# Optimization experiments

Hardware: AMD Instinct MI355X
Metric: run time of the kernel (lower is better)

## Reference

```python
import jax, jax.numpy as jnp
import numpy as np

N, K, A = 4096, 64, 8      # nodes, level-2 paths per node, attrs per l2-neighbor
D = 128                    # embed_dim
NU, NR, NA = 100000, 32, 5000  # user vocab, rating vocab, attribute vocab


def setup_inputs() -> dict:
    key = jax.random.key(0)
    ks = jax.random.split(key, 12)
    s = 0.02
    return dict(
        nodes=jax.random.randint(ks[0], (N,), 0, NU),
        paths_rel=jax.random.randint(ks[1], (N, K, 2), 0, NR),
        paths_nbr=jax.random.randint(ks[2], (N, K), 0, NU),
        attrs=jax.random.randint(ks[3], (N, K, A), 0, NA),
        u2e=jax.random.normal(ks[4], (NU, D), dtype=jnp.float32) * s,
        r2e=jax.random.normal(ks[5], (NR, D), dtype=jnp.float32) * s,
        ua2e=jax.random.normal(ks[6], (NA, D), dtype=jnp.float32) * s,
        W1=jax.random.normal(ks[7], (4 * D, 2 * D), dtype=jnp.float32) * s,
        b1=jnp.zeros((2 * D,), jnp.float32),
        W2=jax.random.normal(ks[8], (2 * D, D), dtype=jnp.float32) * s,
        b2=jnp.zeros((D,), jnp.float32),
        A1=jax.random.normal(ks[9], (2 * D, D), dtype=jnp.float32) * s,
        ab1=jnp.zeros((D,), jnp.float32),
        A2=jax.random.normal(ks[10], (D, D), dtype=jnp.float32) * s,
        ab2=jnp.zeros((D,), jnp.float32),
        A3=jax.random.normal(ks[11], (D, 1), dtype=jnp.float32) * s,
        ab3=jnp.zeros((1,), jnp.float32),
    )


def reference(nodes, paths_rel, paths_nbr, attrs, u2e, r2e, ua2e,
              W1, b1, W2, b2, A1, ab1, A2, ab2, A3, ab3):
    # per-path embedding gathers
    r1 = r2e[paths_rel[..., 0]]           # [N,K,D]
    r2 = r2e[paths_rel[..., 1]]           # [N,K,D]
    ne = u2e[paths_nbr]                   # [N,K,D]
    ae = ua2e[attrs].sum(axis=2)          # [N,K,A,D] -> [N,K,D] (uvAttrEmbedding sum)
    # concat + 2-layer MLP (w_r1, w_r2)
    x = jnp.concatenate([r1, r2, ne, ae], axis=-1)   # [N,K,4D]
    h = jax.nn.relu(x @ W1 + b1)                     # [N,K,2D]
    h = jax.nn.relu(h @ W2 + b2)                     # [N,K,D]
    # attention vs self embedding
    self_e = u2e[nodes]                              # [N,D]
    c = jnp.concatenate(
        [h, jnp.broadcast_to(self_e[:, None, :], h.shape)], axis=-1)  # [N,K,2D]
    a = jax.nn.relu(c @ A1 + ab1)
    a = jax.nn.relu(a @ A2 + ab2)
    logits = (a @ A3 + ab3)[..., 0]                  # [N,K]
    w = jax.nn.softmax(logits, axis=1)
    # attention-weighted reduce over paths
    return jnp.einsum('nk,nkd->nd', w, h)            # [N,D]
```

## Files before the change

### kernel.cpp

```cpp
#include <hip/hip_runtime.h>
#include <hip/hip_bf16.h>

#define NN 4096
#define KK 64
#define AA 8
#define DD 128

#define XH_STRIDE 264
#define A_STRIDE  136
#define H2_STRIDE 136
#define XREG_SZ   16896

typedef __bf16 bf16x8 __attribute__((ext_vector_type(8)));
typedef __bf16 bf16x2 __attribute__((ext_vector_type(2)));
typedef float  f32x4  __attribute__((ext_vector_type(4)));

__device__ __forceinline__ short f2bf(float f) {
    unsigned u = __builtin_bit_cast(unsigned, f);
    u += 0x7FFFu + ((u >> 16) & 1u);
    return (short)(u >> 16);
}
__device__ __forceinline__ float bf2f(short s) {
    unsigned u = ((unsigned)(unsigned short)s) << 16;
    return __builtin_bit_cast(float, u);
}
__device__ __forceinline__ unsigned f2bf2(float a, float b) {
#if __has_builtin(__builtin_amdgcn_cvt_pk_bf16_f32)
    bf16x2 r = __builtin_amdgcn_cvt_pk_bf16_f32(a, b);
    return __builtin_bit_cast(unsigned, r);
#else
    return ((unsigned)(unsigned short)f2bf(a)) | (((unsigned)(unsigned short)f2bf(b)) << 16);
#endif
}
__device__ __forceinline__ void store_bf8(short* dst, float4 a, float4 b) {
    uint4 v;
    v.x = f2bf2(a.x, a.y); v.y = f2bf2(a.z, a.w);
    v.z = f2bf2(b.x, b.y); v.w = f2bf2(b.z, b.w);
    *(uint4*)dst = v;
}

__global__ void prep_all(const float* __restrict__ W1, const float* __restrict__ W2,
                         const float* __restrict__ A1, const float* __restrict__ A2,
                         const int* __restrict__ nodes, const float* __restrict__ u2e,
                         const float* __restrict__ ab1,
                         short* __restrict__ W1p, short* __restrict__ W2p,
                         short* __restrict__ A1p, short* __restrict__ A2p,
                         float* __restrict__ s1g)
{
    if (blockIdx.x < 96) {
        const int t    = blockIdx.x * 256 + threadIdx.x;
        const int idx8 = t * 8;
        const float* src; short* dst; int Ncols, ksl, idx;
        if (idx8 < 131072)      { src = W1; dst = W1p; Ncols = 256; ksl = 4; idx = idx8; }
        else if (idx8 < 163840) { src = W2; dst = W2p; Ncols = 128; ksl = 3; idx = idx8 - 131072; }
        else if (idx8 < 180224) { src = A1; dst = A1p; Ncols = 128; ksl = 2; idx = idx8 - 163840; }
        else                    { src = A2; dst = A2p; Ncols = 128; ksl = 2; idx = idx8 - 180224; }
        const int lane  = (idx >> 3) & 63;
        const int fi    = idx >> 9;
        const int kstep = fi & ((1 << ksl) - 1);
        const int ntile = fi >> ksl;
        const int k0 = kstep * 32 + (lane >> 4) * 8;
        const int nn = ntile * 16 + (lane & 15);
        short v[8];
#pragma unroll
        for (int j = 0; j < 8; ++j)
            v[j] = f2bf(src[(size_t)(k0 + j) * Ncols + nn]);
        *(uint4*)&dst[idx] = *(const uint4*)v;
    } else {
        __shared__ float rows[8][DD];
        const int b = blockIdx.x - 96;
        {
            const int r  = threadIdx.x >> 5;
            const int c4 = (threadIdx.x & 31) * 4;
            const int node = nodes[b * 8 + r];
            *(float4*)&rows[r][c4] = *(const float4*)&u2e[(size_t)node * DD + c4];
        }
        __syncthreads();
        const int h = threadIdx.x >> 7;
        const int c = threadIdx.x & 127;
        const float ab = ab1[c];
        float acc[4] = {ab, ab, ab, ab};
#pragma unroll 4
        for (int i = 0; i < DD; ++i) {
            const float av = A1[(size_t)(DD + i) * DD + c];
#pragma unroll
            for (int j = 0; j < 4; ++j)
                acc[j] = fmaf(rows[h * 4 + j][i], av, acc[j]);
        }
#pragma unroll
        for (int j = 0; j < 4; ++j)
            s1g[(size_t)(b * 8 + h * 4 + j) * DD + c] = acc[j];
    }
}

__global__ void conv_bf16(const float* __restrict__ u2e, const float* __restrict__ r2e,
                          const float* __restrict__ ua2e,
                          short* __restrict__ u2b, short* __restrict__ r2b,
                          short* __restrict__ uab)
{
    const int t  = blockIdx.x * 256 + threadIdx.x;
    const int e8 = t * 8;
    const float* src; short* dst; int off;
    if (e8 < 12800000)      { src = u2e;  dst = u2b; off = e8; }
    else if (e8 < 12804096) { src = r2e;  dst = r2b; off = e8 - 12800000; }
    else if (e8 < 13444096) { src = ua2e; dst = uab; off = e8 - 12804096; }
    else return;
    float4 a = *(const float4*)&src[off];
    float4 b = *(const float4*)&src[off + 4];
    store_bf8(&dst[off], a, b);
}

template<bool BFT>
__launch_bounds__(512, 4)
__global__ void l2agg_mfma(
    const int* __restrict__ paths_rel,
    const int* __restrict__ paths_nbr,
    const int* __restrict__ attrs,
    const float* __restrict__ u2e,
    const float* __restrict__ r2e,
    const float* __restrict__ ua2e,
    const short* __restrict__ u2b,
    const short* __restrict__ r2b,
    const short* __restrict__ uab,
    const float* __restrict__ b1,
    const float* __restrict__ b2,
    const float* __restrict__ ab2,
    const float* __restrict__ A3,
    const float* __restrict__ ab3,
    const short* __restrict__ W1p,
    const short* __restrict__ W2p,
    const short* __restrict__ A1p,
    const short* __restrict__ A2p,
    const float* __restrict__ s1g,
    float* __restrict__ out)
{
    __shared__ short xa[XREG_SZ];
    __shared__ short xb[XREG_SZ];
    __shared__ int   idx_u[576];
    __shared__ float wts8[512];
    float* partials = (float*)idx_u;

    const int n    = blockIdx.x;
    const int tid  = threadIdx.x;
    const int lane = tid & 63;
    const int wv   = tid >> 6;
    const int mr   = lane & 15;
    const int q    = lane >> 4;

    {
        const int* ab = attrs + (size_t)n * KK * AA;
        __builtin_amdgcn_global_load_lds(
            (const __attribute__((address_space(1))) void*)(ab + wv * 64 + lane),
            (__attribute__((address_space(3))) void*)(idx_u + wv * 64), 4, 0, 0);
        if (wv == 0) {
            const int* nb = paths_nbr + (size_t)n * KK;
            __builtin_amdgcn_global_load_lds(
                (const __attribute__((address_space(1))) void*)(nb + lane),
                (__attribute__((address_space(3))) void*)(idx_u + 512), 4, 0, 0);
        }
    }

#pragma unroll
    for (int pass = 0; pass < 2; ++pass) {
        const int p  = pass * 32 + (tid >> 4);
        const int t  = tid & 15;
        const int o  = t * 8;
        const int pk = n * KK + p;
        const int i0 = paths_rel[pk * 2 + 0];
        const int i1 = paths_rel[pk * 2 + 1];
        if constexpr (BFT) {
            uint4 v1 = *(const uint4*)&r2b[(size_t)i0 * DD + o];
            uint4 v2 = *(const uint4*)&r2b[(size_t)i1 * DD + o];
            *(uint4*)&xa[p * XH_STRIDE + o]       = v1;
            *(uint4*)&xa[p * XH_STRIDE + 128 + o] = v2;
        } else {
            float4 r1a = *(const float4*)&r2e[(size_t)i0 * DD + o];
            float4 r1b = *(const float4*)&r2e[(size_t)i0 * DD + o + 4];
            float4 r2a = *(const float4*)&r2e[(size_t)i1 * DD + o];
            float4 r2b_ = *(const float4*)&r2e[(size_t)i1 * DD + o + 4];
            store_bf8(&xa[p * XH_STRIDE + o], r1a, r1b);
            store_bf8(&xa[p * XH_STRIDE + 128 + o], r2a, r2b_);
        }
    }
    __syncthreads();

    const short* W1b = W1p + wv * 2 * 16 * 512 + lane * 8;
    f32x4 acc1[4][2] = {};
    bf16x8 bfc[2], bfn[2];
#pragma unroll
    for (int nt = 0; nt < 2; ++nt) bfc[nt] = *(const bf16x8*)&W1b[nt * 8192];
#pragma unroll
    for (int ks = 0; ks < 8; ++ks) {
#pragma unroll
        for (int nt = 0; nt < 2; ++nt)
            bfn[nt] = *(const bf16x8*)&W1b[nt * 8192 + (ks + 1) * 512];
        bf16x8 af[4];
#pragma unroll
        for (int mt = 0; mt < 4; ++mt)
            af[mt] = *(const bf16x8*)&xa[(mt * 16 + mr) * XH_STRIDE + ks * 32 + q * 8];
#pragma unroll
        for (int nt = 0; nt < 2; ++nt)
#pragma unroll
            for (int mt = 0; mt < 4; ++mt)
                acc1[mt][nt] = __builtin_amdgcn_mfma_f32_16x16x32_bf16(af[mt], bfc[nt], acc1[mt][nt], 0, 0, 0);
#pragma unroll
        for (int nt = 0; nt < 2; ++nt) bfc[nt] = bfn[nt];
    }

    __builtin_amdgcn_sched_barrier(0);

#pragma unroll
    for (int pass = 0; pass < 2; ++pass) {
        const int p  = pass * 32 + (tid >> 4);
        const int t  = tid & 15;
        const int o  = t * 8;
        const int nb = idx_u[512 + p];
        if constexpr (BFT) {
            uint4 nev = *(const uint4*)&u2b[(size_t)nb * DD + o];
            float aes[8] = {0.f, 0.f, 0.f, 0.f, 0.f, 0.f, 0.f, 0.f};
#pragma unroll
            for (int a = 0; a < AA; ++a) {
                const int ai = idx_u[p * AA + a];
                uint4 w = *(const uint4*)&uab[(size_t)ai * DD + o];
                aes[0] += __builtin_bit_cast(float, w.x << 16);
                aes[1] += __builtin_bit_cast(float, w.x & 0xFFFF0000u);
                aes[2] += __builtin_bit_cast(float, w.y << 16);
                aes[3] += __builtin_bit_cast(float, w.y & 0xFFFF0000u);
                aes[4] += __builtin_bit_cast(float, w.z << 16);
                aes[5] += __builtin_bit_cast(float, w.z & 0xFFFF0000u);
                aes[6] += __builtin_bit_cast(float, w.w << 16);
                aes[7] += __builtin_bit_cast(float, w.w & 0xFFFF0000u);
            }
            *(uint4*)&xb[p * XH_STRIDE + o] = nev;
            uint4 pv;
            pv.x = f2bf2(aes[0], aes[1]); pv.y = f2bf2(aes[2], aes[3]);
            pv.z = f2bf2(aes[4], aes[5]); pv.w = f2bf2(aes[6], aes[7]);
            *(uint4*)&xb[p * XH_STRIDE + 128 + o] = pv;
        } else {
            float4 nea = *(const float4*)&u2e[(size_t)nb * DD + o];
            float4 neb = *(const float4*)&u2e[(size_t)nb * DD + o + 4];
            float4 aea = make_float4(0.f, 0.f, 0.f, 0.f);
            float4 aeb = make_float4(0.f, 0.f, 0.f, 0.f);
#pragma unroll
            for (int a = 0; a < AA; ++a) {
                const int ai = idx_u[p * AA + a];
                float4 va = *(const float4*)&ua2e[(size_t)ai * DD + o];
                float4 vb = *(const float4*)&ua2e[(size_t)ai * DD + o + 4];
                aea.x += va.x; aea.y += va.y; aea.z += va.z; aea.w += va.w;
                aeb.x += vb.x; aeb.y += vb.y; aeb.z += vb.z; aeb.w += vb.w;
            }
            store_bf8(&xb[p * XH_STRIDE + o], nea, neb);
            store_bf8(&xb[p * XH_STRIDE + 128 + o], aea, aeb);
        }
    }
    __builtin_amdgcn_sched_barrier(0);
    __syncthreads();

#pragma unroll
    for (int ks = 8; ks < 16; ++ks) {
        if (ks < 15) {
#pragma unroll
            for (int nt = 0; nt < 2; ++nt)
                bfn[nt] = *(const bf16x8*)&W1b[nt * 8192 + (ks + 1) * 512];
        }
        bf16x8 af[4];
#pragma unroll
        for (int mt = 0; mt < 4; ++mt)
            af[mt] = *(const bf16x8*)&xb[(mt * 16 + mr) * XH_STRIDE + (ks - 8) * 32 + q * 8];
#pragma unroll
        for (int nt = 0; nt < 2; ++nt)
#pragma unroll
            for (int mt = 0; mt < 4; ++mt)
                acc1[mt][nt] = __builtin_amdgcn_mfma_f32_16x16x32_bf16(af[mt], bfc[nt], acc1[mt][nt], 0, 0, 0);
        if (ks < 15) {
#pragma unroll
            for (int nt = 0; nt < 2; ++nt) bfc[nt] = bfn[nt];
        }
    }

    const short* W2b = W2p + wv * 8 * 512 + lane * 8;
    bf16x8 g2c = *(const bf16x8*)&W2b[0], g2n;

#pragma unroll
    for (int nt = 0; nt < 2; ++nt) {
        const int col = (wv * 2 + nt) * 16 + mr;
        const float bb = b1[col];
#pragma unroll
        for (int mt = 0; mt < 4; ++mt)
#pragma unroll
            for (int r = 0; r < 4; r += 2) {
                unsigned pk2 = f2bf2(fmaxf(acc1[mt][nt][r] + bb, 0.f),
                                     fmaxf(acc1[mt][nt][r + 1] + bb, 0.f));
                xa[(mt * 16 + q * 4 + r)     * XH_STRIDE + col] = (short)pk2;
                xa[(mt * 16 + q * 4 + r + 1) * XH_STRIDE + col] = (short)(pk2 >> 16);
            }
    }
    __syncthreads();

    f32x4 acc2[4] = {};
#pragma unroll
    for (int ks = 0; ks < 8; ++ks) {
        if (ks < 7) g2n = *(const bf16x8*)&W2b[(ks + 1) * 512];
        bf16x8 af[4];
#pragma unroll
        for (int mt = 0; mt < 4; ++mt)
            af[mt] = *(const bf16x8*)&xa[(mt * 16 + mr) * XH_STRIDE + ks * 32 + q * 8];
#pragma unroll
        for (int mt = 0; mt < 4; ++mt)
            acc2[mt] = __builtin_amdgcn_mfma_f32_16x16x32_bf16(af[mt], g2c, acc2[mt], 0, 0, 0);
        if (ks < 7) g2c = g2n;
    }

    const short* A1b = A1p + wv * 4 * 512 + lane * 8;
    bf16x8 g3f[4];
#pragma unroll
    for (int ks = 0; ks < 4; ++ks) g3f[ks] = *(const bf16x8*)&A1b[ks * 512];
    const float s1v = s1g[(size_t)n * DD + wv * 16 + mr];

    {
        const int col = wv * 16 + mr;
        const float bb = b2[col];
#pragma unroll
        for (int mt = 0; mt < 4; ++mt)
#pragma unroll
            for (int r = 0; r < 4; r += 2) {
                unsigned pk2 = f2bf2(fmaxf(acc2[mt][r] + bb, 0.f),
                                     fmaxf(acc2[mt][r + 1] + bb, 0.f));
                xb[(mt * 16 + q * 4 + r)     * H2_STRIDE + col] = (short)pk2;
                xb[(mt * 16 + q * 4 + r + 1) * H2_STRIDE + col] = (short)(pk2 >> 16);
            }
    }
    __syncthreads();

    {
        f32x4 acc3[4];
#pragma unroll
        for (int mt = 0; mt < 4; ++mt) {
            acc3[mt][0] = s1v; acc3[mt][1] = s1v; acc3[mt][2] = s1v; acc3[mt][3] = s1v;
        }
#pragma unroll
        for (int ks = 0; ks < 4; ++ks) {
            bf16x8 af[4];
#pragma unroll
            for (int mt = 0; mt < 4; ++mt)
                af[mt] = *(const bf16x8*)&xb[(mt * 16 + mr) * H2_STRIDE + ks * 32 + q * 8];
#pragma unroll
            for (int mt = 0; mt < 4; ++mt)
                acc3[mt] = __builtin_amdgcn_mfma_f32_16x16x32_bf16(af[mt], g3f[ks], acc3[mt], 0, 0, 0);
        }
        const short* A2b = A2p + wv * 4 * 512 + lane * 8;
        bf16x8 g4f[4];
#pragma unroll
        for (int ks = 0; ks < 4; ++ks) g4f[ks] = *(const bf16x8*)&A2b[ks * 512];

        {
            const int col = wv * 16 + mr;
#pragma unroll
            for (int mt = 0; mt < 4; ++mt)
#pragma unroll
                for (int r = 0; r < 4; r += 2) {
                    unsigned pk2 = f2bf2(fmaxf(acc3[mt][r], 0.f),
                                         fmaxf(acc3[mt][r + 1], 0.f));
                    xa[(mt * 16 + q * 4 + r)     * A_STRIDE + col] = (short)pk2;
                    xa[(mt * 16 + q * 4 + r + 1) * A_STRIDE + col] = (short)(pk2 >> 16);
                }
        }
        __syncthreads();

        f32x4 acc4[4];
        {
            const float bv = ab2[wv * 16 + mr];
#pragma unroll
            for (int mt = 0; mt < 4; ++mt) {
                acc4[mt][0] = bv; acc4[mt][1] = bv; acc4[mt][2] = bv; acc4[mt][3] = bv;
            }
        }
#pragma unroll
        for (int ks = 0; ks < 4; ++ks) {
            bf16x8 af[4];
#pragma unroll
            for (int mt = 0; mt < 4; ++mt)
                af[mt] = *(const bf16x8*)&xa[(mt * 16 + mr) * A_STRIDE + ks * 32 + q * 8];
#pragma unroll
            for (int mt = 0; mt < 4; ++mt)
                acc4[mt] = __builtin_amdgcn_mfma_f32_16x16x32_bf16(af[mt], g4f[ks], acc4[mt], 0, 0, 0);
        }
        const float av = A3[wv * 16 + mr];
        float pl[4][4];
#pragma unroll
        for (int mt = 0; mt < 4; ++mt)
#pragma unroll
            for (int r = 0; r < 4; ++r)
                pl[mt][r] = fmaxf(acc4[mt][r], 0.f) * av;
#pragma unroll
        for (int off = 1; off < 16; off <<= 1)
#pragma unroll
            for (int mt = 0; mt < 4; ++mt)
#pragma unroll
                for (int r = 0; r < 4; ++r)
                    pl[mt][r] += __shfl_xor(pl[mt][r], off, 64);
        if (mr == 0) {
#pragma unroll
            for (int mt = 0; mt < 4; ++mt)
#pragma unroll
                for (int r = 0; r < 4; ++r)
                    partials[wv * KK + mt * 16 + q * 4 + r] = pl[mt][r];
        }
    }
    __syncthreads();

    {
        float l = ab3[0];
#pragma unroll
        for (int w = 0; w < 8; ++w) l += partials[w * KK + lane];
        float m = l;
#pragma unroll
        for (int off = 32; off > 0; off >>= 1) m = fmaxf(m, __shfl_xor(m, off, 64));
        float e = expf(l - m);
        float s = e;
#pragma unroll
        for (int off = 32; off > 0; off >>= 1) s += __shfl_xor(s, off, 64);
        wts8[wv * 64 + lane] = e / s;
        const int col = wv * 16 + mr;
        const float* wl = &wts8[wv * 64 + q * 16];
        const short* hp = &xb[(q * 16) * H2_STRIDE + col];
        float acc = 0.f;
#pragma unroll
        for (int j = 0; j < 16; ++j)
            acc = fmaf(wl[j], bf2f(hp[j * H2_STRIDE]), acc);
        acc += __shfl_xor(acc, 16, 64);
        acc += __shfl_xor(acc, 32, 64);
        if (q == 0) out[(size_t)n * DD + col] = acc;
    }
}

extern "C" void kernel_launch(void* const* d_in, const int* in_sizes, int n_in,
                              void* d_out, int out_size, void* d_ws, size_t ws_size,
                              hipStream_t stream)
{
    const int*   nodes     = (const int*)d_in[0];
    const int*   paths_rel = (const int*)d_in[1];
    const int*   paths_nbr = (const int*)d_in[2];
    const int*   attrs     = (const int*)d_in[3];
    const float* u2e  = (const float*)d_in[4];
    const float* r2e  = (const float*)d_in[5];
    const float* ua2e = (const float*)d_in[6];
    const float* W1   = (const float*)d_in[7];
    const float* b1   = (const float*)d_in[8];
    const float* W2   = (const float*)d_in[9];
    const float* b2   = (const float*)d_in[10];
    const float* A1   = (const float*)d_in[11];
    const float* ab1  = (const float*)d_in[12];
    const float* A2   = (const float*)d_in[13];
    const float* ab2  = (const float*)d_in[14];
    const float* A3   = (const float*)d_in[15];
    const float* ab3  = (const float*)d_in[16];
    float* out = (float*)d_out;

    short* wsp = (short*)d_ws;
    short* W1p = wsp;
    short* W2p = wsp + 131072;
    short* A1p = wsp + 163840;
    short* A2p = wsp + 180224;
    float* s1g = (float*)((char*)d_ws + 393216);
    short* u2b = (short*)((char*)d_ws + 2490368);
    short* r2b = (short*)((char*)d_ws + 28090368);
    short* uab = (short*)((char*)d_ws + 28098560);

    const size_t WS_NEED = 29378560;
    const bool bft = (ws_size >= WS_NEED);

    prep_all<<<dim3(96 + 512), dim3(256), 0, stream>>>(
        W1, W2, A1, A2, nodes, u2e, ab1, W1p, W2p, A1p, A2p, s1g);
    if (bft) {
        conv_bf16<<<dim3(6565), dim3(256), 0, stream>>>(u2e, r2e, ua2e, u2b, r2b, uab);
        l2agg_mfma<true><<<dim3(NN), dim3(512), 0, stream>>>(
            paths_rel, paths_nbr, attrs, u2e, r2e, ua2e, u2b, r2b, uab,
            b1, b2, ab2, A3, ab3, W1p, W2p, A1p, A2p, s1g, out);
    } else {
        l2agg_mfma<false><<<dim3(NN), dim3(512), 0, stream>>>(
            paths_rel, paths_nbr, attrs, u2e, r2e, ua2e, u2b, r2b, uab,
            b1, b2, ab2, A3, ab3, W1p, W2p, A1p, A2p, s1g, out);
    }
}
```

Before: 274.1 us.

## Merge bf16 table conversion into prep kernel and restructure gather/GEMM ordering

Folds the conv_bf16 table conversion into prep_all as extra blocks, removing one kernel launch. In the main kernel, the attribute indices are loaded with a permuted layout, and paths_rel is read as int2. The neighbour index now comes straight from global memory instead of LDS. The old split, which ran the first half of the W1 GEMM while the second gather was still in flight, is replaced by doing both gathers first and then one 16-step GEMM loop. This loses the overlap of gather latency with MFMA work, and the conversion blocks in prep_all now run even when the workspace is too small.

```diff
diff --git a/kernel.cpp b/kernel.cpp
--- a/kernel.cpp
+++ b/kernel.cpp
@@ -42,10 +42,13 @@
 __global__ void prep_all(const float* __restrict__ W1, const float* __restrict__ W2,
                          const float* __restrict__ A1, const float* __restrict__ A2,
                          const int* __restrict__ nodes, const float* __restrict__ u2e,
+                         const float* __restrict__ r2e, const float* __restrict__ ua2e,
                          const float* __restrict__ ab1,
                          short* __restrict__ W1p, short* __restrict__ W2p,
                          short* __restrict__ A1p, short* __restrict__ A2p,
-                         float* __restrict__ s1g)
+                         float* __restrict__ s1g,
+                         short* __restrict__ u2b, short* __restrict__ r2b,
+                         short* __restrict__ uab)
 {
     if (blockIdx.x < 96) {
         const int t    = blockIdx.x * 256 + threadIdx.x;
@@ -66,7 +69,7 @@
         for (int j = 0; j < 8; ++j)
             v[j] = f2bf(src[(size_t)(k0 + j) * Ncols + nn]);
         *(uint4*)&dst[idx] = *(const uint4*)v;
-    } else {
+    } else if (blockIdx.x < 608) {
         __shared__ float rows[8][DD];
         const int b = blockIdx.x - 96;
         {
@@ -90,24 +93,18 @@
 #pragma unroll
         for (int j = 0; j < 4; ++j)
             s1g[(size_t)(b * 8 + h * 4 + j) * DD + c] = acc[j];
-    }
-}
-
-__global__ void conv_bf16(const float* __restrict__ u2e, const float* __restrict__ r2e,
-                          const float* __restrict__ ua2e,
-                          short* __restrict__ u2b, short* __restrict__ r2b,
-                          short* __restrict__ uab)
-{
-    const int t  = blockIdx.x * 256 + threadIdx.x;
-    const int e8 = t * 8;
-    const float* src; short* dst; int off;
-    if (e8 < 12800000)      { src = u2e;  dst = u2b; off = e8; }
-    else if (e8 < 12804096) { src = r2e;  dst = r2b; off = e8 - 12800000; }
-    else if (e8 < 13444096) { src = ua2e; dst = uab; off = e8 - 12804096; }
-    else return;
-    float4 a = *(const float4*)&src[off];
-    float4 b = *(const float4*)&src[off + 4];
-    store_bf8(&dst[off], a, b);
+    } else {
+        const int t  = (blockIdx.x - 608) * 256 + threadIdx.x;
+        const int e8 = t * 8;
+        const float* src; short* dst; int off;
+        if (e8 < 12800000)      { src = u2e;  dst = u2b; off = e8; }
+        else if (e8 < 12804096) { src = r2e;  dst = r2b; off = e8 - 12800000; }
+        else if (e8 < 13444096) { src = ua2e; dst = uab; off = e8 - 12804096; }
+        else return;
+        float4 a = *(const float4*)&src[off];
+        float4 b = *(const float4*)&src[off + 4];
+        store_bf8(&dst[off], a, b);
+    }
 }
 
 template<bool BFT>
@@ -136,7 +133,7 @@
 {
     __shared__ short xa[XREG_SZ];
     __shared__ short xb[XREG_SZ];
-    __shared__ int   idx_u[576];
+    __shared__ int   idx_u[512];
     __shared__ float wts8[512];
     float* partials = (float*)idx_u;
 
@@ -148,16 +145,13 @@
     const int q    = lane >> 4;
 
     {
+        const int pl = lane >> 3;
+        const int a  = lane & 7;
+        const int p  = wv * 4 + (pl & 3) + (pl >> 2) * 32;
         const int* ab = attrs + (size_t)n * KK * AA;
         __builtin_amdgcn_global_load_lds(
-            (const __attribute__((address_space(1))) void*)(ab + wv * 64 + lane),
-            (__attribute__((address_space(3))) void*)(idx_u + wv * 64), 4, 0, 0);
-        if (wv == 0) {
-            const int* nb = paths_nbr + (size_t)n * KK;
-            __builtin_amdgcn_global_load_lds(
-                (const __attribute__((address_space(1))) void*)(nb + lane),
-                (__attribute__((address_space(3))) void*)(idx_u + 512), 4, 0, 0);
-        }
+            (const __attribute__((address_space(1))) void*)(ab + p * 8 + a),
+            (__attribute__((address_space(3))) void*)(idx_u + wv * 64 + lane), 4, 0, 0);
     }
 
 #pragma unroll
@@ -166,8 +160,9 @@
         const int t  = tid & 15;
         const int o  = t * 8;
         const int pk = n * KK + p;
-        const int i0 = paths_rel[pk * 2 + 0];
-        const int i1 = paths_rel[pk * 2 + 1];
+        const int2 pr = *(const int2*)&paths_rel[pk * 2];
+        const int i0 = pr.x;
+        const int i1 = pr.y;
         if constexpr (BFT) {
             uint4 v1 = *(const uint4*)&r2b[(size_t)i0 * DD + o];
             uint4 v2 = *(const uint4*)&r2b[(size_t)i1 * DD + o];
@@ -182,46 +177,24 @@
             store_bf8(&xa[p * XH_STRIDE + 128 + o], r2a, r2b_);
         }
     }
-    __syncthreads();
-
-    const short* W1b = W1p + wv * 2 * 16 * 512 + lane * 8;
-    f32x4 acc1[4][2] = {};
-    bf16x8 bfc[2], bfn[2];
-#pragma unroll
-    for (int nt = 0; nt < 2; ++nt) bfc[nt] = *(const bf16x8*)&W1b[nt * 8192];
-#pragma unroll
-    for (int ks = 0; ks < 8; ++ks) {
-#pragma unroll
-        for (int nt = 0; nt < 2; ++nt)
-            bfn[nt] = *(const bf16x8*)&W1b[nt * 8192 + (ks + 1) * 512];
-        bf16x8 af[4];
-#pragma unroll
-        for (int mt = 0; mt < 4; ++mt)
-            af[mt] = *(const bf16x8*)&xa[(mt * 16 + mr) * XH_STRIDE + ks * 32 + q * 8];
-#pragma unroll
-        for (int nt = 0; nt < 2; ++nt)
-#pragma unroll
-            for (int mt = 0; mt < 4; ++mt)
-                acc1[mt][nt] = __builtin_amdgcn_mfma_f32_16x16x32_bf16(af[mt], bfc[nt], acc1[mt][nt], 0, 0, 0);
-#pragma unroll
-        for (int nt = 0; nt < 2; ++nt) bfc[nt] = bfn[nt];
-    }
-
-    __builtin_amdgcn_sched_barrier(0);
-
-#pragma unroll
-    for (int pass = 0; pass < 2; ++pass) {
-        const int p  = pass * 32 + (tid >> 4);
+
+    asm volatile("s_waitcnt vmcnt(0)" ::: "memory");
+
+#pragma unroll
+    for (int s = 0; s < 2; ++s) {
+        const int g  = lane >> 4;
+        const int p  = s * 32 + (tid >> 4);
         const int t  = tid & 15;
-        const int o  = t * 8;
-        const int nb = idx_u[512 + p];
+        const int og = t * 8;
+        const int nb = paths_nbr[(size_t)n * KK + p];
+        const int ib = wv * 64 + (s * 4 + g) * 8;
         if constexpr (BFT) {
-            uint4 nev = *(const uint4*)&u2b[(size_t)nb * DD + o];
+            uint4 nev = *(const uint4*)&u2b[(size_t)nb * DD + og];
             float aes[8] = {0.f, 0.f, 0.f, 0.f, 0.f, 0.f, 0.f, 0.f};
 #pragma unroll
             for (int a = 0; a < AA; ++a) {
-                const int ai = idx_u[p * AA + a];
-                uint4 w = *(const uint4*)&uab[(size_t)ai * DD + o];
+                const int ai = idx_u[ib + a];
+                uint4 w = *(const uint4*)&uab[(size_t)ai * DD + og];
                 aes[0] += __builtin_bit_cast(float, w.x << 16);
                 aes[1] += __builtin_bit_cast(float, w.x & 0xFFFF0000u);
                 aes[2] += __builtin_bit_cast(float, w.y << 16);
@@ -231,42 +204,47 @@
                 aes[6] += __builtin_bit_cast(float, w.w << 16);
                 aes[7] += __builtin_bit_cast(float, w.w & 0xFFFF0000u);
             }
-            *(uint4*)&xb[p * XH_STRIDE + o] = nev;
+            *(uint4*)&xb[p * XH_STRIDE + og] = nev;
             uint4 pv;
             pv.x = f2bf2(aes[0], aes[1]); pv.y = f2bf2(aes[2], aes[3]);
             pv.z = f2bf2(aes[4], aes[5]); pv.w = f2bf2(aes[6], aes[7]);
-            *(uint4*)&xb[p * XH_STRIDE + 128 + o] = pv;
+            *(uint4*)&xb[p * XH_STRIDE + 128 + og] = pv;
         } else {
-            float4 nea = *(const float4*)&u2e[(size_t)nb * DD + o];
-            float4 neb = *(const float4*)&u2e[(size_t)nb * DD + o + 4];
+            float4 nea = *(const float4*)&u2e[(size_t)nb * DD + og];
+            float4 neb = *(const float4*)&u2e[(size_t)nb * DD + og + 4];
             float4 aea = make_float4(0.f, 0.f, 0.f, 0.f);
             float4 aeb = make_float4(0.f, 0.f, 0.f, 0.f);
 #pragma unroll
             for (int a = 0; a < AA; ++a) {
-                const int ai = idx_u[p * AA + a];
-                float4 va = *(const float4*)&ua2e[(size_t)ai * DD + o];
-                float4 vb = *(const float4*)&ua2e[(size_t)ai * DD + o + 4];
+                const int ai = idx_u[ib + a];
+                float4 va = *(const float4*)&ua2e[(size_t)ai * DD + og];
+                float4 vb = *(const float4*)&ua2e[(size_t)ai * DD + og + 4];
                 aea.x += va.x; aea.y += va.y; aea.z += va.z; aea.w += va.w;
                 aeb.x += vb.x; aeb.y += vb.y; aeb.z += vb.z; aeb.w += vb.w;
             }
-            store_bf8(&xb[p * XH_STRIDE + o], nea, neb);
-            store_bf8(&xb[p * XH_STRIDE + 128 + o], aea, aeb);
-        }
-    }
-    __builtin_amdgcn_sched_barrier(0);
+            store_bf8(&xb[p * XH_STRIDE + og], nea, neb);
+            store_bf8(&xb[p * XH_STRIDE + 128 + og], aea, aeb);
+        }
+    }
     __syncthreads();
 
-#pragma unroll
-    for (int ks = 8; ks < 16; ++ks) {
+    const short* W1b = W1p + wv * 2 * 16 * 512 + lane * 8;
+    f32x4 acc1[4][2] = {};
+    bf16x8 bfc[2], bfn[2];
+#pragma unroll
+    for (int nt = 0; nt < 2; ++nt) bfc[nt] = *(const bf16x8*)&W1b[nt * 8192];
+#pragma unroll
+    for (int ks = 0; ks < 16; ++ks) {
         if (ks < 15) {
 #pragma unroll
             for (int nt = 0; nt < 2; ++nt)
                 bfn[nt] = *(const bf16x8*)&W1b[nt * 8192 + (ks + 1) * 512];
         }
+        const short* xs = (ks < 8) ? xa : xb;
         bf16x8 af[4];
 #pragma unroll
         for (int mt = 0; mt < 4; ++mt)
-            af[mt] = *(const bf16x8*)&xb[(mt * 16 + mr) * XH_STRIDE + (ks - 8) * 32 + q * 8];
+            af[mt] = *(const bf16x8*)&xs[(mt * 16 + mr) * XH_STRIDE + (ks & 7) * 32 + q * 8];
 #pragma unroll
         for (int nt = 0; nt < 2; ++nt)
 #pragma unroll
@@ -277,6 +255,7 @@
             for (int nt = 0; nt < 2; ++nt) bfc[nt] = bfn[nt];
         }
     }
+    __syncthreads();
 
     const short* W2b = W2p + wv * 8 * 512 + lane * 8;
     bf16x8 g2c = *(const bf16x8*)&W2b[0], g2n;
@@ -470,10 +449,10 @@
     const size_t WS_NEED = 29378560;
     const bool bft = (ws_size >= WS_NEED);
 
-    prep_all<<<dim3(96 + 512), dim3(256), 0, stream>>>(
-        W1, W2, A1, A2, nodes, u2e, ab1, W1p, W2p, A1p, A2p, s1g);
+    prep_all<<<dim3(96 + 512 + 6565), dim3(256), 0, stream>>>(
+        W1, W2, A1, A2, nodes, u2e, r2e, ua2e, ab1,
+        W1p, W2p, A1p, A2p, s1g, u2b, r2b, uab);
     if (bft) {
-        conv_bf16<<<dim3(6565), dim3(256), 0, stream>>>(u2e, r2e, ua2e, u2b, r2b, uab);
         l2agg_mfma<true><<<dim3(NN), dim3(512), 0, stream>>>(
             paths_rel, paths_nbr, attrs, u2e, r2e, ua2e, u2b, r2b, uab,
             b1, b2, ab2, A3, ab3, W1p, W2p, A1p, A2p, s1g, out);
```

Result: slower. 284.0 us (+3.6%).
